# Performance work log

Hardware: AMD Instinct MI355X
Metric: run time of the kernel (lower is better)

## Reference

```python
import jax, jax.numpy as jnp
import numpy as np

B, T, M, L_TP = 32, 4096, 256, 128


def setup_inputs() -> dict:
    key = jax.random.key(0)
    k1, k2, k3, k4 = jax.random.split(key, 4)
    h_1 = jax.random.normal(k1, (B, T, M), dtype=jnp.float32)
    h_2 = jax.random.normal(k2, (B, T, M), dtype=jnp.float32)
    # trunc_normal(mean=-0.1, std=0.1) approximated by clipped normal
    w_tp = jnp.clip(-0.1 + 0.1 * jax.random.normal(k3, (1, L_TP), dtype=jnp.float32), -0.3, 0.1)
    v_tp = jnp.clip(-0.1 + 0.1 * jax.random.normal(k4, (L_TP, M), dtype=jnp.float32), -0.3, 0.1)
    return {"h_1": h_1, "h_2": h_2, "w_tp": w_tp, "v_tp": v_tp}


def reference(h_1, h_2, w_tp, v_tp):
    # Batched over all T timesteps at once (original loops in Python).
    # h: (B, T, 2, M) -- the 2-way stack of the two streams per timestep
    h = jnp.stack([h_1, h_2], axis=2)
    # tanh MLP hidden: (B, T, 2, L_tp)
    temp = jnp.tanh(jnp.einsum('lm,btcm->btcl', v_tp, h))
    # attention logits: (B, T, 2); softmax over the 2-way axis
    scores = jnp.einsum('l,btcl->btc', w_tp[0], temp)
    A = jax.nn.softmax(scores, axis=2)
    # original returns permute of concat (T, 2, B) -> (B, 2, T)
    return jnp.transpose(A, (0, 2, 1))
```

## Files before the change

### kernel.cpp

```cpp
#include <hip/hip_runtime.h>


typedef unsigned short u16;
typedef unsigned int   u32;
typedef __bf16 bf16x8 __attribute__((ext_vector_type(8)));
typedef float  f32x4  __attribute__((ext_vector_type(4)));

union ABFrag { bf16x8 v; u16 u[8]; uint4 q4; };

__device__ __forceinline__ u16 f2bf(float f) {
  u32 u = __float_as_uint(f);
  u += 0x7fffu + ((u >> 16) & 1u);
  return (u16)(u >> 16);
}

__device__ __forceinline__ float fast_tanh(float x) {
  float t = __builtin_amdgcn_exp2f(2.885390082f * x);
  return 1.0f - 2.0f * __builtin_amdgcn_rcpf(t + 1.0f);
}

#define NWG   512
#define ITERS 2

__global__ __launch_bounds__(512, 4) void topo_attn_kernel(
    const float* __restrict__ h1, const float* __restrict__ h2,
    const float* __restrict__ w,  const float* __restrict__ vfp,
    float* __restrict__ out) {
  __shared__ __align__(16) u16 vlds[128 * 256];

  const int tid = threadIdx.x;

  {
    const float4* src = (const float4*)vfp;
    #pragma unroll
    for (int k = 0; k < 8; ++k) {
      int gi = k * 512 + tid;
      float4 f0 = src[gi * 2];
      float4 f1 = src[gi * 2 + 1];
      ABFrag t;
      t.u[0] = f2bf(f0.x); t.u[1] = f2bf(f0.y); t.u[2] = f2bf(f0.z); t.u[3] = f2bf(f0.w);
      t.u[4] = f2bf(f1.x); t.u[5] = f2bf(f1.y); t.u[6] = f2bf(f1.z); t.u[7] = f2bf(f1.w);
      int e0 = gi << 3;
      int l  = e0 >> 8;
      int g  = (e0 & 255) >> 3;
      *(uint4*)&vlds[(l << 8) + (((g + l) & 31) << 3)] = t.q4;
    }
  }
  __syncthreads();

  const int lane = tid & 63;
  const int wave = tid >> 6;
  const int l15  = lane & 15;
  const int q    = lane >> 4;

  float wreg[8];
  #pragma unroll
  for (int lt = 0; lt < 8; ++lt) wreg[lt] = w[lt * 16 + l15];

  #pragma unroll
  for (int it = 0; it < ITERS; ++it) {
    const int wgIter = blockIdx.x + it * NWG;
    const int n0 = (wgIter * 8 + wave) << 4;
    const float4* p1 = (const float4*)(h1 + (size_t)(n0 + l15) * 256) + q * 2;
    const float4* p2 = (const float4*)(h2 + (size_t)(n0 + l15) * 256) + q * 2;

    f32x4 acc0[8], acc1[8];
    #pragma unroll
    for (int lt = 0; lt < 8; ++lt) {
      acc0[lt] = (f32x4){0.f, 0.f, 0.f, 0.f};
      acc1[lt] = (f32x4){0.f, 0.f, 0.f, 0.f};
    }

    #pragma unroll
    for (int ks = 0; ks < 8; ++ks) {
      float4 ra = p1[8 * ks], rb = p1[8 * ks + 1];
      float4 rc = p2[8 * ks], rd = p2[8 * ks + 1];
      ABFrag a1, a2;
      a1.u[0] = f2bf(ra.x); a1.u[1] = f2bf(ra.y); a1.u[2] = f2bf(ra.z); a1.u[3] = f2bf(ra.w);
      a1.u[4] = f2bf(rb.x); a1.u[5] = f2bf(rb.y); a1.u[6] = f2bf(rb.z); a1.u[7] = f2bf(rb.w);
      a2.u[0] = f2bf(rc.x); a2.u[1] = f2bf(rc.y); a2.u[2] = f2bf(rc.z); a2.u[3] = f2bf(rc.w);
      a2.u[4] = f2bf(rd.x); a2.u[5] = f2bf(rd.y); a2.u[6] = f2bf(rd.z); a2.u[7] = f2bf(rd.w);
      #pragma unroll
      for (int lt = 0; lt < 8; ++lt) {
        const int l = (lt << 4) + l15;
        bf16x8 bf = *(const bf16x8*)&vlds[(l << 8) + (((4 * ks + q + l) & 31) << 3)];
        acc0[lt] = __builtin_amdgcn_mfma_f32_16x16x32_bf16(a1.v, bf, acc0[lt], 0, 0, 0);
        acc1[lt] = __builtin_amdgcn_mfma_f32_16x16x32_bf16(a2.v, bf, acc1[lt], 0, 0, 0);
      }
    }

    float s0p[4] = {0.f, 0.f, 0.f, 0.f};
    float s1p[4] = {0.f, 0.f, 0.f, 0.f};
    #pragma unroll
    for (int lt = 0; lt < 8; ++lt) {
      #pragma unroll
      for (int r = 0; r < 4; ++r) {
        s0p[r] += wreg[lt] * fast_tanh(acc0[lt][r]);
        s1p[r] += wreg[lt] * fast_tanh(acc1[lt][r]);
      }
    }
    #pragma unroll
    for (int r = 0; r < 4; ++r) {
      #pragma unroll
      for (int off = 1; off < 16; off <<= 1) {
        s0p[r] += __shfl_xor(s0p[r], off);
        s1p[r] += __shfl_xor(s1p[r], off);
      }
    }
    if (l15 < 4) {
      float s0 = (l15 == 0) ? s0p[0] : (l15 == 1) ? s0p[1] : (l15 == 2) ? s0p[2] : s0p[3];
      float s1 = (l15 == 0) ? s1p[0] : (l15 == 1) ? s1p[1] : (l15 == 2) ? s1p[2] : s1p[3];
      int n = n0 + q * 4 + l15;
      int b = n >> 12, t = n & 4095;
      float e  = __builtin_amdgcn_exp2f(-1.442695041f * (s0 - s1));
      float a0 = __builtin_amdgcn_rcpf(1.0f + e);
      out[b * 8192 + t]        = a0;
      out[b * 8192 + 4096 + t] = 1.0f - a0;
    }
  }
}

extern "C" void kernel_launch(void* const* d_in, const int* in_sizes, int n_in,
                              void* d_out, int out_size, void* d_ws, size_t ws_size,
                              hipStream_t stream) {
  const float* h1 = (const float*)d_in[0];
  const float* h2 = (const float*)d_in[1];
  const float* w  = (const float*)d_in[2];
  const float* v  = (const float*)d_in[3];
  float* out = (float*)d_out;

  topo_attn_kernel<<<NWG, 512, 0, stream>>>(h1, h2, w, v, out);
}
```

Before: 306.4 us.

## Pack both streams into one MFMA tile and software-pipeline global loads

```diff
diff --git a/kernel.cpp b/kernel.cpp
--- a/kernel.cpp
+++ b/kernel.cpp
@@ -19,14 +19,15 @@
   return 1.0f - 2.0f * __builtin_amdgcn_rcpf(t + 1.0f);
 }
 
-#define NWG   512
-#define ITERS 2
+#define NWG     512
+#define ITERS   4
+#define VSTRIDE 264
 
 __global__ __launch_bounds__(512, 4) void topo_attn_kernel(
     const float* __restrict__ h1, const float* __restrict__ h2,
     const float* __restrict__ w,  const float* __restrict__ vfp,
     float* __restrict__ out) {
-  __shared__ __align__(16) u16 vlds[128 * 256];
+  __shared__ __align__(16) u16 vlds[128 * VSTRIDE];
 
   const int tid = threadIdx.x;
 
@@ -40,10 +41,9 @@
       ABFrag t;
       t.u[0] = f2bf(f0.x); t.u[1] = f2bf(f0.y); t.u[2] = f2bf(f0.z); t.u[3] = f2bf(f0.w);
       t.u[4] = f2bf(f1.x); t.u[5] = f2bf(f1.y); t.u[6] = f2bf(f1.z); t.u[7] = f2bf(f1.w);
-      int e0 = gi << 3;
-      int l  = e0 >> 8;
-      int g  = (e0 & 255) >> 3;
-      *(uint4*)&vlds[(l << 8) + (((g + l) & 31) << 3)] = t.q4;
+      int l = gi >> 5;
+      int g = gi & 31;
+      *(uint4*)&vlds[l * VSTRIDE + g * 8] = t.q4;
     }
   }
   __syncthreads();
@@ -57,62 +57,67 @@
   #pragma unroll
   for (int lt = 0; lt < 8; ++lt) wreg[lt] = w[lt * 16 + l15];
 
+  const int row8 = l15 & 7;
+  const float* hbase = (l15 < 8) ? h1 : h2;
+  const int n0base = blockIdx.x * 64 + wave * 8;
+  const float4* p = (const float4*)(hbase + (size_t)(n0base + row8) * 256) + q * 2;
+
+  int vbase[8];
+  #pragma unroll
+  for (int lt = 0; lt < 8; ++lt)
+    vbase[lt] = ((lt * 16 + l15) * VSTRIDE + q * 8) * 2;
+
+  float4 bufA[3], bufB[3];
+  bufA[0] = p[0]; bufB[0] = p[1];
+  bufA[1] = p[8]; bufB[1] = p[9];
+
   #pragma unroll
   for (int it = 0; it < ITERS; ++it) {
-    const int wgIter = blockIdx.x + it * NWG;
-    const int n0 = (wgIter * 8 + wave) << 4;
-    const float4* p1 = (const float4*)(h1 + (size_t)(n0 + l15) * 256) + q * 2;
-    const float4* p2 = (const float4*)(h2 + (size_t)(n0 + l15) * 256) + q * 2;
-
-    f32x4 acc0[8], acc1[8];
+    f32x4 acc[8];
     #pragma unroll
-    for (int lt = 0; lt < 8; ++lt) {
-      acc0[lt] = (f32x4){0.f, 0.f, 0.f, 0.f};
-      acc1[lt] = (f32x4){0.f, 0.f, 0.f, 0.f};
-    }
+    for (int lt = 0; lt < 8; ++lt) acc[lt] = (f32x4){0.f, 0.f, 0.f, 0.f};
 
     #pragma unroll
     for (int ks = 0; ks < 8; ++ks) {
-      float4 ra = p1[8 * ks], rb = p1[8 * ks + 1];
-      float4 rc = p2[8 * ks], rd = p2[8 * ks + 1];
-      ABFrag a1, a2;
-      a1.u[0] = f2bf(ra.x); a1.u[1] = f2bf(ra.y); a1.u[2] = f2bf(ra.z); a1.u[3] = f2bf(ra.w);
-      a1.u[4] = f2bf(rb.x); a1.u[5] = f2bf(rb.y); a1.u[6] = f2bf(rb.z); a1.u[7] = f2bf(rb.w);
-      a2.u[0] = f2bf(rc.x); a2.u[1] = f2bf(rc.y); a2.u[2] = f2bf(rc.z); a2.u[3] = f2bf(rc.w);
-      a2.u[4] = f2bf(rd.x); a2.u[5] = f2bf(rd.y); a2.u[6] = f2bf(rd.z); a2.u[7] = f2bf(rd.w);
+      const int s = it * 8 + ks;
+      if (s + 2 < ITERS * 8) {
+        const int s2  = s + 2;
+        const int it2 = s2 >> 3, ks2 = s2 & 7;
+        const float4* pp = p + it2 * 2097152 + ks2 * 8;
+        bufA[s2 % 3] = pp[0];
+        bufB[s2 % 3] = pp[1];
+      }
+      float4 fa = bufA[s % 3], fb = bufB[s % 3];
+      ABFrag a;
+      a.u[0] = f2bf(fa.x); a.u[1] = f2bf(fa.y); a.u[2] = f2bf(fa.z); a.u[3] = f2bf(fa.w);
+      a.u[4] = f2bf(fb.x); a.u[5] = f2bf(fb.y); a.u[6] = f2bf(fb.z); a.u[7] = f2bf(fb.w);
       #pragma unroll
       for (int lt = 0; lt < 8; ++lt) {
-        const int l = (lt << 4) + l15;
-        bf16x8 bf = *(const bf16x8*)&vlds[(l << 8) + (((4 * ks + q + l) & 31) << 3)];
-        acc0[lt] = __builtin_amdgcn_mfma_f32_16x16x32_bf16(a1.v, bf, acc0[lt], 0, 0, 0);
-        acc1[lt] = __builtin_amdgcn_mfma_f32_16x16x32_bf16(a2.v, bf, acc1[lt], 0, 0, 0);
+        bf16x8 bfr = *(const bf16x8*)((const char*)vlds + (vbase[lt] + ks * 64));
+        acc[lt] = __builtin_amdgcn_mfma_f32_16x16x32_bf16(a.v, bfr, acc[lt], 0, 0, 0);
       }
     }
 
-    float s0p[4] = {0.f, 0.f, 0.f, 0.f};
-    float s1p[4] = {0.f, 0.f, 0.f, 0.f};
+    float s_p[4] = {0.f, 0.f, 0.f, 0.f};
     #pragma unroll
     for (int lt = 0; lt < 8; ++lt) {
       #pragma unroll
-      for (int r = 0; r < 4; ++r) {
-        s0p[r] += wreg[lt] * fast_tanh(acc0[lt][r]);
-        s1p[r] += wreg[lt] * fast_tanh(acc1[lt][r]);
-      }
+      for (int r = 0; r < 4; ++r)
+        s_p[r] += wreg[lt] * fast_tanh(acc[lt][r]);
     }
     #pragma unroll
     for (int r = 0; r < 4; ++r) {
       #pragma unroll
-      for (int off = 1; off < 16; off <<= 1) {
-        s0p[r] += __shfl_xor(s0p[r], off);
-        s1p[r] += __shfl_xor(s1p[r], off);
-      }
+      for (int off = 1; off < 16; off <<= 1)
+        s_p[r] += __shfl_xor(s_p[r], off);
     }
-    if (l15 < 4) {
-      float s0 = (l15 == 0) ? s0p[0] : (l15 == 1) ? s0p[1] : (l15 == 2) ? s0p[2] : s0p[3];
-      float s1 = (l15 == 0) ? s1p[0] : (l15 == 1) ? s1p[1] : (l15 == 2) ? s1p[2] : s1p[3];
-      int n = n0 + q * 4 + l15;
+    const int r = l15 & 3;
+    float sel = (r == 0) ? s_p[0] : (r == 1) ? s_p[1] : (r == 2) ? s_p[2] : s_p[3];
+    float oth = __shfl_xor(sel, 32);
+    if (q < 2 && l15 < 4) {
+      int n = n0base + it * 32768 + q * 4 + l15;
       int b = n >> 12, t = n & 4095;
-      float e  = __builtin_amdgcn_exp2f(-1.442695041f * (s0 - s1));
+      float e  = __builtin_amdgcn_exp2f(-1.442695041f * (sel - oth));
       float a0 = __builtin_amdgcn_rcpf(1.0f + e);
       out[b * 8192 + t]        = a0;
       out[b * 8192 + 4096 + t] = 1.0f - a0;
```

Measured after the change: 287.5 us. 1.07x faster.
